# Performance work log

Measured on AMD Instinct MI355X. Metric: run time of the kernel, lower is better.

The kernel has to match this reference:

```python
import jax, jax.numpy as jnp
import numpy as np

VOC_QUANT = (32, 32, 32)   # voc_size = 32768
EMB_QUANT = (8, 8, 16)     # emb_size = 1024
RANKS = (1, 8, 8, 1)       # TT-ranks
PADDING_IDX = 0
EMB_SIZE = int(np.prod(EMB_QUANT))


def setup_inputs() -> dict:
    key = jax.random.key(0)
    k0, k1, k2, kx = jax.random.split(key, 4)
    x = jax.random.randint(kx, (8, 4096), 0, int(np.prod(VOC_QUANT)), dtype=jnp.int64)
    # cores stored as [voc_quant_k, r_{k-1}, emb_quant_k, r_k]
    def core(k, n, rp, e, r):
        std = (2.0 / (rp * e * r)) ** 0.5  # glorot-ish scale per core
        return jax.random.normal(k, (n, rp, e, r), dtype=jnp.float32) * std
    core0 = core(k0, VOC_QUANT[0], RANKS[0], EMB_QUANT[0], RANKS[1])
    core1 = core(k1, VOC_QUANT[1], RANKS[1], EMB_QUANT[1], RANKS[2])
    core2 = core(k2, VOC_QUANT[2], RANKS[2], EMB_QUANT[2], RANKS[3])
    return {"x": x, "core0": core0, "core1": core1, "core2": core2}


def reference(x, core0, core1, core2):
    xshape = x.shape
    flat = x.reshape(-1)                       # [N]
    N = flat.shape[0]
    # ind2sub: row-major decomposition of flat index over VOC_QUANT
    strides = (VOC_QUANT[1] * VOC_QUANT[2], VOC_QUANT[2], 1)
    idx = [(flat // s) % q for s, q in zip(strides, VOC_QUANT)]
    # gather rows from each core: g_k has shape [N, r_{k-1}, e_k, r_k]
    g0 = jnp.take(core0, idx[0], axis=0)
    g1 = jnp.take(core1, idx[1], axis=0)
    g2 = jnp.take(core2, idx[2], axis=0)
    # full(): chain of small batched contractions over the TT-ranks
    res = g0.reshape(N, EMB_QUANT[0], RANKS[1])                 # r_{-1}=1
    res = jnp.einsum('ner,nrfs->nefs', res, g1).reshape(
        N, EMB_QUANT[0] * EMB_QUANT[1], RANKS[2])
    res = jnp.einsum('ner,nrfs->nefs', res, g2).reshape(N, EMB_SIZE)  # r_d=1
    # padding mask
    res = jnp.where((flat != PADDING_IDX)[:, None], res, 0.0)
    return res.reshape(*xshape, EMB_SIZE)
```

## Files before the change

kernel.cpp:

```cpp
#include <hip/hip_runtime.h>


__global__ __launch_bounds__(256) void tt_emb_kernel(
    const int* __restrict__ x,
    const float* __restrict__ c0,
    const float* __restrict__ c1,
    const float* __restrict__ c2,
    float* __restrict__ out)
{
    const int n = blockIdx.x;
    const int t = threadIdx.x;

    __shared__ float s0[64];
    __shared__ float s1[512];
    __shared__ float s2[128];

    const int flat = x[n];
    const int i0 = (flat >> 10) & 31;
    const int i1 = (flat >> 5) & 31;
    const int i2 = flat & 31;

    if (t < 64)  s0[t] = c0[i0 * 64 + t];
    s1[t]        = c1[i1 * 512 + t];
    s1[t + 256]  = c1[i1 * 512 + 256 + t];
    if (t < 128) s2[t] = c2[i2 * 128 + t];
    __syncthreads();

    const int e0  = t >> 5;
    const int e1  = (t >> 2) & 7;
    const int e2b = (t & 3) << 2;

    float tmp[8] = {0.f, 0.f, 0.f, 0.f, 0.f, 0.f, 0.f, 0.f};
    #pragma unroll
    for (int r1 = 0; r1 < 8; ++r1) {
        const float a = s0[e0 * 8 + r1];
        #pragma unroll
        for (int r2 = 0; r2 < 8; ++r2)
            tmp[r2] = fmaf(a, s1[r1 * 64 + e1 * 8 + r2], tmp[r2]);
    }

    float res[4];
    #pragma unroll
    for (int q = 0; q < 4; ++q) {
        float acc = 0.f;
        #pragma unroll
        for (int r2 = 0; r2 < 8; ++r2)
            acc = fmaf(tmp[r2], s2[r2 * 16 + e2b + q], acc);
        res[q] = acc;
    }

    if (flat == 0) { res[0] = res[1] = res[2] = res[3] = 0.f; }

    float4 o = make_float4(res[0], res[1], res[2], res[3]);
    *reinterpret_cast<float4*>(out + (size_t)n * 1024 + (size_t)t * 4) = o;
}

extern "C" void kernel_launch(void* const* d_in, const int* in_sizes, int n_in,
                              void* d_out, int out_size, void* d_ws, size_t ws_size,
                              hipStream_t stream) {
    const int*   x  = (const int*)d_in[0];
    const float* c0 = (const float*)d_in[1];
    const float* c1 = (const float*)d_in[2];
    const float* c2 = (const float*)d_in[3];
    float* out = (float*)d_out;

    const int N = in_sizes[0];
    tt_emb_kernel<<<N, 256, 0, stream>>>(x, c0, c1, c2, out);
}
```

Before: 39.45 us.

## Precompute core0×core1 products into workspace table and contract with core2 directly

Adds a pre-pass kernel that contracts every (i0,i1) pair of core0 and core1 into a 1024×512 table in workspace. The main kernel then loads its 8-element slice from that table and does only the final rank-8 contraction with core2, with no LDS staging or __syncthreads. This removes the per-token first contraction and the shared-memory barrier. In exchange it adds a second launch and a 2 MB table write and read. The old LDS kernel remains as a fallback when the workspace is too small.

```diff
diff --git a/kernel.cpp b/kernel.cpp
--- a/kernel.cpp
+++ b/kernel.cpp
@@ -1,7 +1,74 @@
 #include <hip/hip_runtime.h>
 
 
+#define TT_A_BYTES (1024u * 512u * 4u)
+
+__global__ __launch_bounds__(256) void tt_precomp_kernel(
+    const float* __restrict__ c0,
+    const float* __restrict__ c1,
+    float* __restrict__ A)
+{
+    const int i0 = blockIdx.x >> 5;
+    const int i1 = blockIdx.x & 31;
+    const float* c0r = c0 + i0 * 64;
+    const float* c1r = c1 + i1 * 512;
+    float* Ar = A + (size_t)blockIdx.x * 512;
+
+    #pragma unroll
+    for (int v = threadIdx.x; v < 512; v += 256) {
+        const int pair = v >> 3;
+        const int r2   = v & 7;
+        const int e0   = pair >> 3;
+        const int e1   = pair & 7;
+        float acc = 0.f;
+        #pragma unroll
+        for (int r1 = 0; r1 < 8; ++r1)
+            acc = fmaf(c0r[e0 * 8 + r1], c1r[r1 * 64 + e1 * 8 + r2], acc);
+        Ar[v] = acc;
+    }
+}
+
 __global__ __launch_bounds__(256) void tt_emb_kernel(
+    const int* __restrict__ x,
+    const float* __restrict__ A,
+    const float* __restrict__ c2,
+    float* __restrict__ out)
+{
+    const int n = blockIdx.x;
+    const int t = threadIdx.x;
+
+    const int flat = x[n];
+    const int i0 = (flat >> 10) & 31;
+    const int i1 = (flat >> 5) & 31;
+    const int i2 = flat & 31;
+
+    const float* Ar  = A + ((size_t)(i0 * 32 + i1)) * 512;
+    const float* c2r = c2 + i2 * 128;
+
+    const int pair = t >> 2;
+    const int e2b  = (t & 3) << 2;
+
+    const float4 tlo = *reinterpret_cast<const float4*>(Ar + pair * 8);
+    const float4 thi = *reinterpret_cast<const float4*>(Ar + pair * 8 + 4);
+    const float tmp[8] = {tlo.x, tlo.y, tlo.z, tlo.w, thi.x, thi.y, thi.z, thi.w};
+
+    float r0 = 0.f, r1 = 0.f, r2v = 0.f, r3 = 0.f;
+    #pragma unroll
+    for (int r = 0; r < 8; ++r) {
+        const float4 cv = *reinterpret_cast<const float4*>(c2r + r * 16 + e2b);
+        r0 = fmaf(tmp[r], cv.x, r0);
+        r1 = fmaf(tmp[r], cv.y, r1);
+        r2v = fmaf(tmp[r], cv.z, r2v);
+        r3 = fmaf(tmp[r], cv.w, r3);
+    }
+
+    if (flat == 0) { r0 = r1 = r2v = r3 = 0.f; }
+
+    *reinterpret_cast<float4*>(out + (size_t)n * 1024 + (size_t)t * 4) =
+        make_float4(r0, r1, r2v, r3);
+}
+
+__global__ __launch_bounds__(256) void tt_emb_lds_kernel(
     const int* __restrict__ x,
     const float* __restrict__ c0,
     const float* __restrict__ c1,
@@ -51,8 +118,8 @@
 
     if (flat == 0) { res[0] = res[1] = res[2] = res[3] = 0.f; }
 
-    float4 o = make_float4(res[0], res[1], res[2], res[3]);
-    *reinterpret_cast<float4*>(out + (size_t)n * 1024 + (size_t)t * 4) = o;
+    *reinterpret_cast<float4*>(out + (size_t)n * 1024 + (size_t)t * 4) =
+        make_float4(res[0], res[1], res[2], res[3]);
 }
 
 extern "C" void kernel_launch(void* const* d_in, const int* in_sizes, int n_in,
@@ -65,5 +132,12 @@
     float* out = (float*)d_out;
 
     const int N = in_sizes[0];
-    tt_emb_kernel<<<N, 256, 0, stream>>>(x, c0, c1, c2, out);
+
+    if (ws_size >= TT_A_BYTES) {
+        float* A = (float*)d_ws;
+        tt_precomp_kernel<<<1024, 256, 0, stream>>>(c0, c1, A);
+        tt_emb_kernel<<<N, 256, 0, stream>>>(x, A, c2, out);
+    } else {
+        tt_emb_lds_kernel<<<N, 256, 0, stream>>>(x, c0, c1, c2, out);
+    }
 }
```

Result: slower. 53.24 us (+35.0%).
